# Kernel tuning notes

Measured on AMD Instinct MI355X. Metric: run time of the kernel, lower is better.

The kernel has to match this reference:

```python
import jax, jax.numpy as jnp
import numpy as np

B, N, D, S = 128, 512, 256, 8


def setup_inputs() -> dict:
    key = jax.random.key(0)
    k1, k2, k3, k4, k5, k6, k7 = jax.random.split(key, 7)
    node_feat = jax.random.normal(k1, (B, N, D), dtype=jnp.float32)
    query = jax.random.normal(k2, (B, D), dtype=jnp.float32)
    edge_matrices = jax.random.uniform(k3, (B, N, N), dtype=jnp.float32)
    att_stack = jax.random.uniform(k4, (B, N, S), dtype=jnp.float32)
    # soft one-hot stack pointer (as produced by the controller in the original model)
    ptr_idx = jax.random.randint(k5, (B,), 1, S)
    stack_ptr = jax.nn.one_hot(ptr_idx, S, dtype=jnp.float32)
    value_mem = jnp.zeros((B, N), dtype=jnp.float32)
    W = jax.random.normal(k6, (D, D), dtype=jnp.float32) * 0.02  # nn.Linear weight [out,in]
    b = jnp.zeros((D,), dtype=jnp.float32)
    return {
        "node_feat": node_feat, "query": query, "edge_matrices": edge_matrices,
        "att_stack": att_stack, "stack_ptr": stack_ptr, "value_mem": value_mem,
        "W": W, "b": b,
    }


def reference(node_feat, query, edge_matrices, att_stack, stack_ptr, value_mem, W, b):
    # read_from_stack: weighted sum over stack depth -> key attention [B, N]
    key_attn = jnp.sum(att_stack * stack_ptr[:, None, :], axis=-1)
    # attention-weighted node feature [B, D] and adjacency row [B, N]
    key_feat = jnp.sum(node_feat * key_attn[:, :, None], axis=1)
    edge_matrix = jnp.sum(edge_matrices * key_attn[:, :, None], axis=1)
    # linear projection of key feature -> query vector [B, D]
    q = key_feat @ W.T + b
    # neighbors = node_feat * edge_matrix[..., None]; logits = neighbors @ q
    logits = jnp.einsum('bnd,bn,bd->bn', node_feat, edge_matrix, q)
    # write_to_stack with zero attention: zero out the slot under the pointer
    new_att_stack = att_stack * (1.0 - stack_ptr[:, None, :])
    # _move_ptr_bw: shift pointer toward stack bottom; bottom absorbs itself
    shifted = jnp.concatenate([stack_ptr[:, 1:], jnp.zeros((stack_ptr.shape[0], 1), stack_ptr.dtype)], axis=1)
    new_stack_ptr = shifted.at[:, 0].add(stack_ptr[:, 0])
    new_value_mem = value_mem + logits
    return (new_att_stack, new_stack_ptr, new_value_mem)
```

## Files before the change

### kernel.cpp

```cpp
#include <hip/hip_runtime.h>

#define B 128
#define N 512
#define D 256
#define S 8

typedef float f32x4 __attribute__((ext_vector_type(4)));

__global__ __launch_bounds__(256) void k1_fused(
    const float* __restrict__ node, const float* __restrict__ edge,
    const float* __restrict__ att, const float* __restrict__ spi,
    float* __restrict__ out_att, float* __restrict__ out_sp,
    float* __restrict__ kf, float* __restrict__ em) {
    const int b = blockIdx.y;
    const int role = blockIdx.x;
    const int tid = threadIdx.x;
    __shared__ float sps[S];
    __shared__ float kal[64];
    if (tid < S) sps[tid] = spi[b * S + tid];
    __syncthreads();

    if (role < 8) {
        const int i0 = role * 64;
        if (tid < 64) {
            const float4* a = reinterpret_cast<const float4*>(att + ((size_t)(b * N + i0 + tid)) * S);
            float4 a0 = a[0], a1 = a[1];
            kal[tid] = a0.x * sps[0] + a0.y * sps[1] + a0.z * sps[2] + a0.w * sps[3]
                     + a1.x * sps[4] + a1.y * sps[5] + a1.z * sps[6] + a1.w * sps[7];
        }
        __syncthreads();
        const int r = tid >> 7;
        const int c = tid & 127;
        const float4* base = reinterpret_cast<const float4*>(edge + ((size_t)(b * N + i0)) * N)
                           + (size_t)r * (N / 4) + c;
        float4 acc = make_float4(0.f, 0.f, 0.f, 0.f);
        float4 v[8];
        for (int dr0 = 0; dr0 < 32; dr0 += 8) {
            #pragma unroll
            for (int u = 0; u < 8; ++u) v[u] = base[(size_t)(dr0 + u) * 2 * (N / 4)];
            #pragma unroll
            for (int u = 0; u < 8; ++u) {
                float k = kal[(dr0 + u) * 2 + r];
                acc.x += k * v[u].x; acc.y += k * v[u].y;
                acc.z += k * v[u].z; acc.w += k * v[u].w;
            }
        }
        float* dst = em + b * N + c * 4;
        unsafeAtomicAdd(dst + 0, acc.x);
        unsafeAtomicAdd(dst + 1, acc.y);
        unsafeAtomicAdd(dst + 2, acc.z);
        unsafeAtomicAdd(dst + 3, acc.w);
    } else {
        const int n0 = (role - 8) * 64;
        __shared__ float4 red[256];
        if (tid < 64) {
            const float4* a = reinterpret_cast<const float4*>(att + ((size_t)(b * N + n0 + tid)) * S);
            float4 a0 = a[0], a1 = a[1];
            kal[tid] = a0.x * sps[0] + a0.y * sps[1] + a0.z * sps[2] + a0.w * sps[3]
                     + a1.x * sps[4] + a1.y * sps[5] + a1.z * sps[6] + a1.w * sps[7];
            f32x4 o0 = {a0.x * (1.f - sps[0]), a0.y * (1.f - sps[1]),
                        a0.z * (1.f - sps[2]), a0.w * (1.f - sps[3])};
            f32x4 o1 = {a1.x * (1.f - sps[4]), a1.y * (1.f - sps[5]),
                        a1.z * (1.f - sps[6]), a1.w * (1.f - sps[7])};
            f32x4* oa = reinterpret_cast<f32x4*>(out_att + ((size_t)(b * N + n0 + tid)) * S);
            __builtin_nontemporal_store(o0, &oa[0]);
            __builtin_nontemporal_store(o1, &oa[1]);
        }
        if (role == 8 && tid < S) {
            float v = (tid < S - 1) ? sps[tid + 1] : 0.0f;
            if (tid == 0) v += sps[0];
            out_sp[b * S + tid] = v;
        }
        __syncthreads();
        const int r = tid >> 6;
        const int c = tid & 63;
        const float4* base = reinterpret_cast<const float4*>(node + ((size_t)(b * N + n0)) * D)
                           + (size_t)r * (D / 4) + c;
        float4 acc = make_float4(0.f, 0.f, 0.f, 0.f);
        float4 v[8];
        for (int j0 = 0; j0 < 16; j0 += 8) {
            #pragma unroll
            for (int u = 0; u < 8; ++u) v[u] = base[(size_t)(j0 + u) * 4 * (D / 4)];
            #pragma unroll
            for (int u = 0; u < 8; ++u) {
                float k = kal[(j0 + u) * 4 + r];
                acc.x += k * v[u].x; acc.y += k * v[u].y;
                acc.z += k * v[u].z; acc.w += k * v[u].w;
            }
        }
        red[tid] = acc;
        __syncthreads();
        if (tid < 64) {
            float4 a0 = red[c], a1 = red[c + 64], a2 = red[c + 128], a3 = red[c + 192];
            float4 s = make_float4(a0.x + a1.x + a2.x + a3.x,
                                   a0.y + a1.y + a2.y + a3.y,
                                   a0.z + a1.z + a2.z + a3.z,
                                   a0.w + a1.w + a2.w + a3.w);
            float* dst = kf + b * D + c * 4;
            unsafeAtomicAdd(dst + 0, s.x);
            unsafeAtomicAdd(dst + 1, s.y);
            unsafeAtomicAdd(dst + 2, s.z);
            unsafeAtomicAdd(dst + 3, s.w);
        }
    }
}

__global__ void kC_q(const float* __restrict__ Wm,
                     const float* __restrict__ bias,
                     const float* __restrict__ kf,
                     float* __restrict__ q) {
    const int b = blockIdx.x;
    const int d = threadIdx.x;
    __shared__ float kfl[D];
    kfl[d] = kf[b * D + d];
    __syncthreads();
    float acc = bias[d];
    const float4* wrow = reinterpret_cast<const float4*>(Wm + (size_t)d * D);
    const float4* kf4 = reinterpret_cast<const float4*>(kfl);
    float4 w[8];
    for (int k0 = 0; k0 < D / 4; k0 += 8) {
        #pragma unroll
        for (int u = 0; u < 8; ++u) w[u] = wrow[k0 + u];
        #pragma unroll
        for (int u = 0; u < 8; ++u) {
            float4 f = kf4[k0 + u];
            acc += w[u].x * f.x + w[u].y * f.y + w[u].z * f.z + w[u].w * f.w;
        }
    }
    q[b * D + d] = acc;
}

__global__ void kD_logits(const float* __restrict__ node,
                          const float* __restrict__ em,
                          const float* __restrict__ q,
                          const float* __restrict__ vm,
                          float* __restrict__ out_vm) {
    const int row0 = blockIdx.x * 32;
    const int b = row0 / N;
    const int tid = threadIdx.x;
    const int wave = tid >> 6;
    const int lane = tid & 63;
    __shared__ float ql[D];
    if (tid < D) ql[tid] = q[b * D + tid];
    __syncthreads();
    const float4 q4 = reinterpret_cast<const float4*>(ql)[lane];
    const int wr0 = row0 + wave * 8;
    float emv = 0.f, vmv = 0.f;
    if (lane < 8) {
        emv = em[wr0 + lane];
        vmv = vm[wr0 + lane];
    }
    float4 v[8];
    #pragma unroll
    for (int r = 0; r < 8; ++r)
        v[r] = reinterpret_cast<const float4*>(node + (size_t)(wr0 + r) * D)[lane];
    float myS = 0.f;
    #pragma unroll
    for (int r = 0; r < 8; ++r) {
        float s = v[r].x * q4.x + v[r].y * q4.y + v[r].z * q4.z + v[r].w * q4.w;
        #pragma unroll
        for (int off = 32; off; off >>= 1) s += __shfl_xor(s, off);
        if (lane == r) myS = s;
    }
    if (lane < 8) {
        out_vm[wr0 + lane] = vmv + emv * myS;
    }
}

extern "C" void kernel_launch(void* const* d_in, const int* in_sizes, int n_in,
                              void* d_out, int out_size, void* d_ws, size_t ws_size,
                              hipStream_t stream) {
    const float* node = (const float*)d_in[0];
    const float* edge = (const float*)d_in[2];
    const float* att  = (const float*)d_in[3];
    const float* sp   = (const float*)d_in[4];
    const float* vm   = (const float*)d_in[5];
    const float* Wm   = (const float*)d_in[6];
    const float* bias = (const float*)d_in[7];

    float* out_att = (float*)d_out;
    float* out_sp  = out_att + (size_t)B * N * S;
    float* out_vm  = out_sp + (size_t)B * S;

    float* ws = (float*)d_ws;
    float* kf = ws;
    float* em = kf + (size_t)B * D;
    float* q  = em + (size_t)B * N;

    (void)hipMemsetAsync(kf, 0, (size_t)(B * D + B * N) * sizeof(float), stream);

    k1_fused<<<dim3(16, B), 256, 0, stream>>>(node, edge, att, sp,
                                              out_att, out_sp, kf, em);
    kC_q<<<B, D, 0, stream>>>(Wm, bias, kf, q);
    kD_logits<<<(B * N) / 32, 256, 0, stream>>>(node, em, q, vm, out_vm);
}
```

Before: 65.79 us.

## Stage edge and node tiles into LDS via async global_load_lds double buffering

Replaces direct register loads of edge and node tiles in the fused reduction kernel with asynchronous global-to-LDS copies (global_load_lds) into a double-buffered shared-memory ring. Explicit vmcnt waits and barriers overlap the next tile's fetch with the current tile's accumulation. The logits kernel also stages its node rows through LDS instead of loading them into registers. This adds 32KB of LDS per block, which can lower occupancy, plus extra barrier traffic. On a purely bandwidth-bound workload the async-copy path may not beat plain vectorized loads.

```diff
diff --git a/kernel.cpp b/kernel.cpp
--- a/kernel.cpp
+++ b/kernel.cpp
@@ -6,6 +6,14 @@
 #define S 8
 
 typedef float f32x4 __attribute__((ext_vector_type(4)));
+
+#define GLOBAL_AS __attribute__((address_space(1)))
+#define LDS_AS    __attribute__((address_space(3)))
+
+__device__ __forceinline__ void stage16(const float* g, float* l) {
+    __builtin_amdgcn_global_load_lds((const GLOBAL_AS void*)g,
+                                     (LDS_AS void*)l, 16, 0, 0);
+}
 
 __global__ __launch_bounds__(256) void k1_fused(
     const float* __restrict__ node, const float* __restrict__ edge,
@@ -15,8 +23,13 @@
     const int b = blockIdx.y;
     const int role = blockIdx.x;
     const int tid = threadIdx.x;
+    const int lane = tid & 63;
+    const int w = tid >> 6;
+
+    __shared__ float sm[8192];
+    __shared__ float kal[64];
     __shared__ float sps[S];
-    __shared__ float kal[64];
+
     if (tid < S) sps[tid] = spi[b * S + tid];
     __syncthreads();
 
@@ -29,21 +42,45 @@
                      + a1.x * sps[4] + a1.y * sps[5] + a1.z * sps[6] + a1.w * sps[7];
         }
         __syncthreads();
+
+        const float* gbase = edge + ((size_t)b * N + i0) * N;
+        float* stA = sm;
+        float* stB = sm + 4096;
         const int r = tid >> 7;
         const int c = tid & 127;
-        const float4* base = reinterpret_cast<const float4*>(edge + ((size_t)(b * N + i0)) * N)
-                           + (size_t)r * (N / 4) + c;
-        float4 acc = make_float4(0.f, 0.f, 0.f, 0.f);
-        float4 v[8];
-        for (int dr0 = 0; dr0 < 32; dr0 += 8) {
+
+        {
+            const float* g0 = gbase + w * 1024 + lane * 4;
+            float* l0 = stA + w * 1024;
+            stage16(g0 + 0,   l0 + 0);
+            stage16(g0 + 256, l0 + 256);
+            stage16(g0 + 512, l0 + 512);
+            stage16(g0 + 768, l0 + 768);
+        }
+        f32x4 acc = {0.f, 0.f, 0.f, 0.f};
+        for (int t = 0; t < 8; ++t) {
+            const int h = t & 1;
+            if (t < 7) {
+                const float* g = gbase + (t + 1) * 4096 + w * 1024 + lane * 4;
+                float* l = (h ? stA : stB) + w * 1024;
+                stage16(g + 0,   l + 0);
+                stage16(g + 256, l + 256);
+                stage16(g + 512, l + 512);
+                stage16(g + 768, l + 768);
+                asm volatile("s_waitcnt vmcnt(4)" ::: "memory");
+            } else {
+                asm volatile("s_waitcnt vmcnt(0)" ::: "memory");
+            }
+            __builtin_amdgcn_sched_barrier(0);
+            __builtin_amdgcn_s_barrier();
+            const f32x4* lb4 = reinterpret_cast<const f32x4*>(h ? stB : stA);
             #pragma unroll
-            for (int u = 0; u < 8; ++u) v[u] = base[(size_t)(dr0 + u) * 2 * (N / 4)];
-            #pragma unroll
-            for (int u = 0; u < 8; ++u) {
-                float k = kal[(dr0 + u) * 2 + r];
-                acc.x += k * v[u].x; acc.y += k * v[u].y;
-                acc.z += k * v[u].z; acc.w += k * v[u].w;
-            }
+            for (int k = 0; k < 4; ++k) {
+                float kv = kal[t * 8 + 2 * k + r];
+                acc += kv * lb4[(2 * k + r) * 128 + c];
+            }
+            __builtin_amdgcn_sched_barrier(0);
+            __builtin_amdgcn_s_barrier();
         }
         float* dst = em + b * N + c * 4;
         unsafeAtomicAdd(dst + 0, acc.x);
@@ -52,7 +89,6 @@
         unsafeAtomicAdd(dst + 3, acc.w);
     } else {
         const int n0 = (role - 8) * 64;
-        __shared__ float4 red[256];
         if (tid < 64) {
             const float4* a = reinterpret_cast<const float4*>(att + ((size_t)(b * N + n0 + tid)) * S);
             float4 a0 = a[0], a1 = a[1];
@@ -72,30 +108,46 @@
             out_sp[b * S + tid] = v;
         }
         __syncthreads();
-        const int r = tid >> 6;
+
+        const float* gbase = node + ((size_t)b * N + n0) * D;
+        float* stA = sm;
+        float* stB = sm + 2048;
         const int c = tid & 63;
-        const float4* base = reinterpret_cast<const float4*>(node + ((size_t)(b * N + n0)) * D)
-                           + (size_t)r * (D / 4) + c;
-        float4 acc = make_float4(0.f, 0.f, 0.f, 0.f);
-        float4 v[8];
-        for (int j0 = 0; j0 < 16; j0 += 8) {
+
+        {
+            const float* g0 = gbase + w * 512 + lane * 4;
+            float* l0 = stA + w * 512;
+            stage16(g0 + 0,   l0 + 0);
+            stage16(g0 + 256, l0 + 256);
+        }
+        f32x4 acc = {0.f, 0.f, 0.f, 0.f};
+        for (int t = 0; t < 8; ++t) {
+            const int h = t & 1;
+            if (t < 7) {
+                const float* g = gbase + (t + 1) * 2048 + w * 512 + lane * 4;
+                float* l = (h ? stA : stB) + w * 512;
+                stage16(g + 0,   l + 0);
+                stage16(g + 256, l + 256);
+                asm volatile("s_waitcnt vmcnt(2)" ::: "memory");
+            } else {
+                asm volatile("s_waitcnt vmcnt(0)" ::: "memory");
+            }
+            __builtin_amdgcn_sched_barrier(0);
+            __builtin_amdgcn_s_barrier();
+            const f32x4* lb4 = reinterpret_cast<const f32x4*>(h ? stB : stA);
             #pragma unroll
-            for (int u = 0; u < 8; ++u) v[u] = base[(size_t)(j0 + u) * 4 * (D / 4)];
-            #pragma unroll
-            for (int u = 0; u < 8; ++u) {
-                float k = kal[(j0 + u) * 4 + r];
-                acc.x += k * v[u].x; acc.y += k * v[u].y;
-                acc.z += k * v[u].z; acc.w += k * v[u].w;
-            }
-        }
+            for (int k = 0; k < 2; ++k) {
+                float kv = kal[t * 8 + 4 * k + w];
+                acc += kv * lb4[(4 * k + w) * 64 + c];
+            }
+            __builtin_amdgcn_sched_barrier(0);
+            __builtin_amdgcn_s_barrier();
+        }
+        f32x4* red = reinterpret_cast<f32x4*>(sm + 4096);
         red[tid] = acc;
         __syncthreads();
         if (tid < 64) {
-            float4 a0 = red[c], a1 = red[c + 64], a2 = red[c + 128], a3 = red[c + 192];
-            float4 s = make_float4(a0.x + a1.x + a2.x + a3.x,
-                                   a0.y + a1.y + a2.y + a3.y,
-                                   a0.z + a1.z + a2.z + a3.z,
-                                   a0.w + a1.w + a2.w + a3.w);
+            f32x4 s = red[c] + red[c + 64] + red[c + 128] + red[c + 192];
             float* dst = kf + b * D + c * 4;
             unsafeAtomicAdd(dst + 0, s.x);
             unsafeAtomicAdd(dst + 1, s.y);
@@ -130,34 +182,43 @@
     q[b * D + d] = acc;
 }
 
-__global__ void kD_logits(const float* __restrict__ node,
-                          const float* __restrict__ em,
-                          const float* __restrict__ q,
-                          const float* __restrict__ vm,
-                          float* __restrict__ out_vm) {
+__global__ __launch_bounds__(256) void kD_logits(
+    const float* __restrict__ node,
+    const float* __restrict__ em,
+    const float* __restrict__ q,
+    const float* __restrict__ vm,
+    float* __restrict__ out_vm) {
     const int row0 = blockIdx.x * 32;
     const int b = row0 / N;
     const int tid = threadIdx.x;
     const int wave = tid >> 6;
     const int lane = tid & 63;
     __shared__ float ql[D];
+    __shared__ float sm[8192];
     if (tid < D) ql[tid] = q[b * D + tid];
     __syncthreads();
     const float4 q4 = reinterpret_cast<const float4*>(ql)[lane];
     const int wr0 = row0 + wave * 8;
+
+    float* myl = sm + wave * 2048;
+    const float* g0 = node + (size_t)wr0 * D + lane * 4;
+    #pragma unroll
+    for (int r = 0; r < 8; ++r)
+        stage16(g0 + (size_t)r * D, myl + r * 256);
+
     float emv = 0.f, vmv = 0.f;
     if (lane < 8) {
         emv = em[wr0 + lane];
         vmv = vm[wr0 + lane];
     }
-    float4 v[8];
-    #pragma unroll
-    for (int r = 0; r < 8; ++r)
-        v[r] = reinterpret_cast<const float4*>(node + (size_t)(wr0 + r) * D)[lane];
+    asm volatile("s_waitcnt vmcnt(0)" ::: "memory");
+    __builtin_amdgcn_sched_barrier(0);
+
     float myS = 0.f;
     #pragma unroll
     for (int r = 0; r < 8; ++r) {
-        float s = v[r].x * q4.x + v[r].y * q4.y + v[r].z * q4.z + v[r].w * q4.w;
+        const f32x4 v = reinterpret_cast<const f32x4*>(myl + r * 256)[lane];
+        float s = v.x * q4.x + v.y * q4.y + v.z * q4.z + v.w * q4.w;
         #pragma unroll
         for (int off = 32; off; off >>= 1) s += __shfl_xor(s, off);
         if (lane == r) myS = s;
```

After: 69.37 us. +5.4%, slower.
